# Kernel tuning notes

Measured on AMD Instinct MI355X. Metric: run time of the kernel, lower is better.

## Reference

```python
import jax, jax.numpy as jnp
import numpy as np

B, T, N, DIN = 16, 40, 64, 64
H = 256          # n_hid == msg_out == gru_hid (required by the module's own shape constraints)
MSG_HID = 256
DOUT = 64
E = N * (N - 1)  # fully-connected directed graph, no self loops


def _linear_params(key, fin, fout):
    kw, kb = jax.random.split(key)
    s = 1.0 / np.sqrt(fin)
    w = jax.random.uniform(kw, (fout, fin), minval=-s, maxval=s, dtype=jnp.float32)
    b = jax.random.uniform(kb, (fout,), minval=-s, maxval=s, dtype=jnp.float32)
    return w, b


def setup_inputs() -> dict:
    key = jax.random.key(0)
    ks = jax.random.split(key, 16)
    # one-hot incidence matrices for all ordered node pairs (i != j)
    pairs = np.array([(i, j) for i in range(N) for j in range(N) if i != j])
    eye = np.eye(N, dtype=np.float32)
    rel_send = jnp.asarray(eye[pairs[:, 0]])  # [E, N]
    rel_rec = jnp.asarray(eye[pairs[:, 1]])   # [E, N]

    inputs = jax.random.normal(ks[0], (B, T, N, DIN), dtype=jnp.float32)
    rel_types = jax.random.uniform(ks[1], (B, E, 2), dtype=jnp.float32)

    d = {"inputs": inputs, "rel_rec": rel_rec, "rel_send": rel_send, "rel_types": rel_types}
    names_dims = [
        ("msg_fc1", 2 * H, MSG_HID), ("msg_fc2", MSG_HID, H),
        ("gru_ir", DIN, H), ("gru_hr", H, H),
        ("gru_ii", DIN, H), ("gru_hi", H, H),
        ("gru_in", DIN, H), ("gru_hn", H, H),
        ("out_fc1", H, H), ("out_fc2", H, H), ("out_fc3", H, DOUT),
    ]
    for k, (name, fin, fout) in zip(ks[2:13], names_dims):
        w, b = _linear_params(k, fin, fout)
        d[name + "_w"] = w
        d[name + "_b"] = b
    return d


def _lin(x, w, b):
    return x @ w.T + b


def reference(inputs, rel_rec, rel_send, rel_types,
              msg_fc1_w, msg_fc1_b, msg_fc2_w, msg_fc2_b,
              gru_ir_w, gru_ir_b, gru_hr_w, gru_hr_b,
              gru_ii_w, gru_ii_b, gru_hi_w, gru_hi_b,
              gru_in_w, gru_in_b, gru_hn_w, gru_hn_b,
              out_fc1_w, out_fc1_b, out_fc2_w, out_fc2_b, out_fc3_w, out_fc3_b):
    b, t, n, _ = inputs.shape
    # both edge-type branches share the same message MLP, so the summed
    # message equals msg * (rel_types[...,0] + rel_types[...,1])
    type_sum = rel_types[:, :, 0:1] + rel_types[:, :, 1:2]  # [B, E, 1]

    def step(hidden, xt):
        # node2edge on hidden: [B, E, 2H]
        senders = jnp.einsum('en,bnh->beh', rel_send, hidden)
        receivers = jnp.einsum('en,bnh->beh', rel_rec, hidden)
        pre_msg = jnp.concatenate([senders, receivers], axis=-1)
        msg = jax.nn.relu(_lin(pre_msg, msg_fc1_w, msg_fc1_b))
        msg = jax.nn.relu(_lin(msg, msg_fc2_w, msg_fc2_b))
        all_msgs = msg * type_sum                                   # [B, E, H]
        agg_msgs = jnp.einsum('beh,en->bnh', all_msgs, rel_rec)     # edge2node
        r = jax.nn.sigmoid(_lin(xt, gru_ir_w, gru_ir_b) + _lin(agg_msgs, gru_hr_w, gru_hr_b))
        i = jax.nn.sigmoid(_lin(xt, gru_ii_w, gru_ii_b) + _lin(agg_msgs, gru_hi_w, gru_hi_b))
        nn_ = jnp.tanh(_lin(xt, gru_in_w, gru_in_b) + r * _lin(agg_msgs, gru_hn_w, gru_hn_b))
        hidden = (1.0 - i) * nn_ + i * hidden
        pred = jax.nn.relu(_lin(hidden, out_fc1_w, out_fc1_b))
        pred = jax.nn.relu(_lin(pred, out_fc2_w, out_fc2_b))
        pred = _lin(pred, out_fc3_w, out_fc3_b)
        return hidden, pred

    xs = jnp.transpose(inputs[:, :-1], (1, 0, 2, 3))  # time-major [T-1, B, N, DIN]
    h0 = jnp.zeros((b, n, H), dtype=inputs.dtype)
    _, preds = jax.lax.scan(step, h0, xs)
    return jnp.transpose(preds, (1, 0, 2, 3))          # [B, T-1, N, n_out]
```

## Files before the change

### kernel.cpp

```cpp
#include <hip/hip_runtime.h>
#include <math.h>


namespace {
constexpr int kB = 16, kT = 40, kTS = 39, kN = 64, kDin = 64, kH = 256;
constexpr int kE = kN * (kN - 1);
constexpr int kBN = kB * kN;
constexpr int kDout = 64;
}

typedef _Float16 half8 __attribute__((ext_vector_type(8)));
typedef short short8 __attribute__((ext_vector_type(8)));
typedef float f32x4 __attribute__((ext_vector_type(4)));

__device__ __forceinline__ float sigm(float x) { return 1.f / (1.f + expf(-x)); }

__device__ __forceinline__ unsigned short f2h(float x) {
    _Float16 h = (_Float16)x;
    return __builtin_bit_cast(unsigned short, h);
}

__device__ __forceinline__ uint4 pack8h(const float* x) {
    unsigned us[8];
    #pragma unroll
    for (int q = 0; q < 8; ++q) us[q] = f2h(x[q]);
    uint4 p;
    p.x = us[0] | (us[1] << 16); p.y = us[2] | (us[3] << 16);
    p.z = us[4] | (us[5] << 16); p.w = us[6] | (us[7] << 16);
    return p;
}

__global__ void setup_kernel(
    const float* __restrict__ rel_rec, const float* __restrict__ rel_send,
    const float* __restrict__ rel_types, const float* __restrict__ W2,
    const float* __restrict__ Whr, const float* __restrict__ Whi,
    const float* __restrict__ Whn, const float* __restrict__ Wir,
    const float* __restrict__ Wii, const float* __restrict__ Win,
    const float* __restrict__ W1,
    const float* __restrict__ bir, const float* __restrict__ bhr,
    const float* __restrict__ bii, const float* __restrict__ bhi,
    const float* __restrict__ fc1w, const float* __restrict__ fc2w,
    const float* __restrict__ fc3w,
    int* __restrict__ edge_at, float* __restrict__ ts,
    unsigned short* __restrict__ W2f,
    unsigned short* __restrict__ Wri,
    unsigned short* __restrict__ Wnh,
    unsigned short* __restrict__ Wnx,
    unsigned short* __restrict__ Wuv,
    unsigned short* __restrict__ F1, unsigned short* __restrict__ F2,
    unsigned short* __restrict__ F3,
    float* __restrict__ bri) {
    int idx = blockIdx.x * 256 + threadIdx.x;
    if (idx < kE) {
        int si = 0, ri = 0;
        for (int n = 0; n < kN; ++n) {
            if (rel_send[idx * kN + n] > 0.5f) si = n;
            if (rel_rec[idx * kN + n] > 0.5f) ri = n;
        }
        edge_at[ri * kN + si] = idx;
    }
    if (idx < kB * kE) ts[idx] = rel_types[2 * idx] + rel_types[2 * idx + 1];
    if (idx < kH * kH) {
        W2f[idx] = f2h(W2[idx]);
        Wnh[idx] = f2h(Whn[idx]);
        F1[idx] = f2h(fc1w[idx]);
        F2[idx] = f2h(fc2w[idx]);
    }
    if (idx < 512 * 320) {
        int row = idx / 320, k = idx - row * 320;
        float v;
        if (row < 256) v = (k < kH) ? Whr[row * kH + k] : Wir[row * kDin + k - kH];
        else { int o = row - 256; v = (k < kH) ? Whi[o * kH + k] : Wii[o * kDin + k - kH]; }
        Wri[idx] = f2h(v);
    }
    if (idx < kH * kDin) Wnx[idx] = f2h(Win[idx]);
    if (idx < 512 * 256) {
        int row = idx >> 8, k = idx & 255;
        float v = (row < 256) ? W1[row * 512 + k] : W1[(row - 256) * 512 + 256 + k];
        Wuv[idx] = f2h(v);
    }
    if (idx < kDout * kH) F3[idx] = f2h(fc3w[idx]);
    if (idx < 256) bri[idx] = bir[idx] + bhr[idx];
    else if (idx < 512) bri[idx] = bii[idx - 256] + bhi[idx - 256];
}

__global__ __launch_bounds__(512, 1)
void step_kernel(const float* __restrict__ hprev,
                 const float* __restrict__ inputs, int t,
                 const float* __restrict__ Uin, const float* __restrict__ Vin,
                 const unsigned short* __restrict__ W2f,
                 const float* __restrict__ b1, const float* __restrict__ b2,
                 const float* __restrict__ ts, const int* __restrict__ edge_at,
                 const unsigned short* __restrict__ Wri,
                 const unsigned short* __restrict__ Wnh,
                 const unsigned short* __restrict__ Wnx,
                 const unsigned short* __restrict__ Wuv,
                 const float* __restrict__ bri, const float* __restrict__ bhn,
                 const float* __restrict__ bin_,
                 float* __restrict__ hnew,
                 float* __restrict__ Uo, float* __restrict__ Vo,
                 unsigned short* __restrict__ hist16) {
    __shared__ __align__(16) unsigned short h1[kN * kH];
    __shared__ float vjb4[4][kH];
    __shared__ float tss4[4][kN];
    __shared__ float aggL[4][kH];
    __shared__ __align__(16) unsigned short Zf[16 * 320];
    __shared__ __align__(16) unsigned short Hf[16 * 256];

    const int tid = threadIdx.x;
    const int lane = tid & 63, w = tid >> 6;
    const int mrow = lane & 15, mq = lane >> 4;
    const int cb = ((blockIdx.x & 7) << 5) | (blockIdx.x >> 3);
    const int m0 = cb * 4;
    const int b = cb >> 4, j0 = (cb & 15) * 4;

    {
        const int jj = tid >> 7, o = tid & 127;
        const int j = j0 + jj;
        vjb4[jj][o] = Vin[(size_t)(b * kN + j) * kH + o] + b1[o];
        vjb4[jj][o + 128] = Vin[(size_t)(b * kN + j) * kH + o + 128] + b1[o + 128];
        if (o < kN) {
            int e = edge_at[j * kN + o];
            tss4[jj][o] = (e < 0) ? 0.f : ts[b * kE + e];
        }
    }

    const int uo = tid & 31, ui0 = tid >> 5;
    float ur[4][8];
    #pragma unroll
    for (int p = 0; p < 4; ++p) {
        const float4* up = (const float4*)(Uin + (size_t)(b * kN + ui0 + 16 * p) * kH + uo * 8);
        *(float4*)&ur[p][0] = up[0];
        *(float4*)&ur[p][4] = up[1];
    }

    const unsigned short* Wp = W2f + (size_t)(w * 32 + mrow) * kH + mq * 8;
    half8 bb[8][2];
    #pragma unroll
    for (int kt = 0; kt < 8; ++kt)
        #pragma unroll
        for (int nf = 0; nf < 2; ++nf)
            bb[kt][nf] = *(const half8*)(Wp + nf * 16 * kH + kt * 32);
    __builtin_amdgcn_sched_barrier(0);
    __syncthreads();

    #pragma unroll 1
    for (int jj = 0; jj < 4; ++jj) {
        const int j = j0 + jj;
        {
            const int k0 = uo * 8;
            float vj[8];
            *(float4*)&vj[0] = *(const float4*)&vjb4[jj][k0];
            *(float4*)&vj[4] = *(const float4*)&vjb4[jj][k0 + 4];
            #pragma unroll
            for (int p = 0; p < 4; ++p) {
                const int i = ui0 + 16 * p;
                float x[8];
                #pragma unroll
                for (int q = 0; q < 8; ++q)
                    x[q] = (i == j) ? 0.f : fmaxf(ur[p][q] + vj[q], 0.f);
                const int byte = i * 512 + ((k0 * 2) ^ ((i & 7) << 4));
                *(uint4*)((char*)h1 + byte) = pack8h(x);
            }
        }
        __syncthreads();

        f32x4 acc[4][2];
        #pragma unroll
        for (int mf = 0; mf < 4; ++mf)
            #pragma unroll
            for (int nf = 0; nf < 2; ++nf) acc[mf][nf] = (f32x4){0.f, 0.f, 0.f, 0.f};
        #pragma unroll
        for (int kt = 0; kt < 8; ++kt) {
            const int k0 = kt * 32;
            half8 a[4];
            #pragma unroll
            for (int mf = 0; mf < 4; ++mf) {
                const int r = mf * 16 + mrow;
                const int byte = r * 512 + (((k0 + mq * 8) * 2) ^ ((r & 7) << 4));
                a[mf] = *(const half8*)((const char*)h1 + byte);
            }
            #pragma unroll
            for (int mf = 0; mf < 4; ++mf)
                #pragma unroll
                for (int nf = 0; nf < 2; ++nf)
                    acc[mf][nf] = __builtin_amdgcn_mfma_f32_16x16x32_f16(
                        a[mf], bb[kt][nf], acc[mf][nf], 0, 0, 0);
        }

        float tsr[16];
        #pragma unroll
        for (int mf = 0; mf < 4; ++mf)
            #pragma unroll
            for (int r = 0; r < 4; ++r)
                tsr[mf * 4 + r] = tss4[jj][mf * 16 + mq * 4 + r];
        #pragma unroll
        for (int nf = 0; nf < 2; ++nf) {
            const int col = w * 32 + nf * 16 + mrow;
            const float bv = b2[col];
            float s = 0.f;
            #pragma unroll
            for (int mf = 0; mf < 4; ++mf)
                #pragma unroll
                for (int r = 0; r < 4; ++r)
                    s += tsr[mf * 4 + r] * fmaxf(acc[mf][nf][r] + bv, 0.f);
            s += __shfl_xor(s, 16);
            s += __shfl_xor(s, 32);
            if (lane < 16) aggL[jj][col] = s;
        }
        __syncthreads();
    }

    {
        const uint4 z4 = {0u, 0u, 0u, 0u};
        for (int c = tid; c < 4 * 40; c += 512) {
            const int r = c / 40, g = c - r * 40;
            float x[8];
            if (g < 32) {
                #pragma unroll
                for (int q = 0; q < 8; ++q) x[q] = aggL[r][g * 8 + q];
            } else {
                const int grow = m0 + r, bb_ = grow >> 6, n = grow & 63;
                const float* xp = inputs + ((size_t)(bb_ * kT + t) * kN + n) * kDin + (g - 32) * 8;
                *(float4*)&x[0] = ((const float4*)xp)[0];
                *(float4*)&x[4] = ((const float4*)xp)[1];
            }
            const int byte = r * 640 + ((g ^ (r & 7)) << 4);
            *(uint4*)((char*)Zf + byte) = pack8h(x);
        }
        for (int c = tid; c < 12 * 40; c += 512) {
            const int r = 4 + c / 40, g = c - (c / 40) * 40;
            const int byte = r * 640 + ((g ^ (r & 7)) << 4);
            *(uint4*)((char*)Zf + byte) = z4;
        }
        for (int c = tid; c < 12 * 32; c += 512) {
            const int r = 4 + c / 32, g = c & 31;
            const int byte = r * 512 + ((g ^ (r & 7)) << 4);
            *(uint4*)((char*)Hf + byte) = z4;
        }
    }
    __syncthreads();

    #pragma unroll
    for (int nf = 0; nf < 2; ++nf) {
        const int col = w * 32 + nf * 16 + mrow;
        const unsigned short* WR = Wri + (size_t)col * 320 + mq * 8;
        const unsigned short* WI = Wri + (size_t)(256 + col) * 320 + mq * 8;
        const unsigned short* WNh = Wnh + (size_t)col * kH + mq * 8;
        const unsigned short* WNx = Wnx + (size_t)col * kDin + mq * 8;

        half8 rwa[10][3];
        #pragma unroll
        for (int kt = 0; kt < 10; ++kt) {
            rwa[kt][0] = *(const half8*)(WR + kt * 32);
            rwa[kt][1] = *(const half8*)(WI + kt * 32);
            if (kt < 8) rwa[kt][2] = *(const half8*)(WNh + kt * 32);
            else        rwa[kt][2] = *(const half8*)(WNx + (kt * 32 - 256));
        }
        __builtin_amdgcn_sched_barrier(0);

        f32x4 aR = {0.f,0.f,0.f,0.f}, aI = {0.f,0.f,0.f,0.f};
        f32x4 aNH = {0.f,0.f,0.f,0.f}, aNX = {0.f,0.f,0.f,0.f};
        #pragma unroll
        for (int kt = 0; kt < 10; ++kt) {
            const int g = kt * 4 + mq;
            const int byte = mrow * 640 + ((g ^ (mrow & 7)) << 4);
            half8 zf = *(const half8*)((const char*)Zf + byte);
            aR = __builtin_amdgcn_mfma_f32_16x16x32_f16(zf, rwa[kt][0], aR, 0, 0, 0);
            aI = __builtin_amdgcn_mfma_f32_16x16x32_f16(zf, rwa[kt][1], aI, 0, 0, 0);
            if (kt < 8) aNH = __builtin_amdgcn_mfma_f32_16x16x32_f16(zf, rwa[kt][2], aNH, 0, 0, 0);
            else        aNX = __builtin_amdgcn_mfma_f32_16x16x32_f16(zf, rwa[kt][2], aNX, 0, 0, 0);
        }

        if (mq == 0) {
            const float brv = bri[col], biv = bri[256 + col];
            const float bhnv = bhn[col], binv = bin_[col];
            #pragma unroll
            for (int reg = 0; reg < 4; ++reg) {
                const int lr = reg;
                const int grow = m0 + lr;
                float rg = sigm(aR[reg] + brv);
                float ig = sigm(aI[reg] + biv);
                float ng = tanhf(aNX[reg] + binv + rg * (aNH[reg] + bhnv));
                float h2 = (1.f - ig) * ng + ig * hprev[(size_t)grow * kH + col];
                hnew[(size_t)grow * kH + col] = h2;
                const unsigned short hv = f2h(h2);
                __builtin_nontemporal_store(
                    hv, &hist16[((size_t)t * kBN + grow) * kH + col]);
                const int byte = lr * 512 + (((col >> 3) ^ (lr & 7)) << 4) + (col & 7) * 2;
                *(unsigned short*)((char*)Hf + byte) = hv;
            }
        }
    }
    __syncthreads();

    #pragma unroll
    for (int nf = 0; nf < 4; ++nf) {
        const int col = w * 64 + nf * 16 + mrow;
        const unsigned short* Wp2 = Wuv + (size_t)col * kH + mq * 8;
        half8 rwa[8];
        #pragma unroll
        for (int kt = 0; kt < 8; ++kt) rwa[kt] = *(const half8*)(Wp2 + kt * 32);
        __builtin_amdgcn_sched_barrier(0);
        f32x4 aUV = {0.f, 0.f, 0.f, 0.f};
        #pragma unroll
        for (int kt = 0; kt < 8; ++kt) {
            const int g = kt * 4 + mq;
            const int byte = mrow * 512 + ((g ^ (mrow & 7)) << 4);
            half8 zf = *(const half8*)((const char*)Hf + byte);
            aUV = __builtin_amdgcn_mfma_f32_16x16x32_f16(zf, rwa[kt], aUV, 0, 0, 0);
        }
        if (mq == 0) {
            #pragma unroll
            for (int reg = 0; reg < 4; ++reg) {
                const int grow = m0 + reg;
                const float v = aUV[reg];
                if (col < 256) Uo[(size_t)grow * kH + col] = v;
                else Vo[(size_t)grow * kH + col - 256] = v;
            }
        }
    }
}

__global__ __launch_bounds__(256, 2)
void out_kernel(const unsigned short* __restrict__ hist16,
                const unsigned short* __restrict__ F1,
                const unsigned short* __restrict__ F2,
                const unsigned short* __restrict__ F3,
                const float* __restrict__ fc1b, const float* __restrict__ fc2b,
                const float* __restrict__ fc3b, float* __restrict__ out) {
    __shared__ __align__(16) unsigned short Af[64 * 256];
    __shared__ __align__(16) unsigned short Bf[64 * 256];
    const int m0 = blockIdx.x * 64;
    const int tid = threadIdx.x;
    const int lane = tid & 63, w = tid >> 6;
    const int mrow = lane & 15, mq = lane >> 4;

    #pragma unroll
    for (int it = 0; it < 8; ++it) {
        const int c = tid + it * 256;
        const int r = c >> 5, o = c & 31;
        short8 v = *(const short8*)(hist16 + (size_t)(m0 + r) * kH + o * 8);
        const int byte = r * 512 + ((o << 4) ^ ((r & 7) << 4));
        *(short8*)((char*)Af + byte) = v;
    }
    __syncthreads();

    #define LAYER(SRC, WW, BIAS, DST)                                           \
    {                                                                           \
        const unsigned short* wb = WW + (size_t)(w * 64 + mrow) * kH + mq * 8;  \
        half8 wall[8][4];                                                       \
        _Pragma("unroll")                                                       \
        for (int kt = 0; kt < 8; ++kt)                                          \
            _Pragma("unroll")                                                   \
            for (int nf = 0; nf < 4; ++nf)                                      \
                wall[kt][nf] = *(const half8*)(wb + nf * 16 * kH + kt * 32);    \
        __builtin_amdgcn_sched_barrier(0);                                      \
        f32x4 acc[4][4];                                                        \
        _Pragma("unroll")                                                       \
        for (int m = 0; m < 4; ++m)                                             \
            _Pragma("unroll")                                                   \
            for (int nf = 0; nf < 4; ++nf) acc[m][nf] = (f32x4){0.f,0.f,0.f,0.f};\
        _Pragma("unroll")                                                       \
        for (int kt = 0; kt < 8; ++kt) {                                        \
            const int k0 = kt * 32;                                             \
            half8 zf[4];                                                        \
            _Pragma("unroll")                                                   \
            for (int m = 0; m < 4; ++m) {                                       \
                const int r = m * 16 + mrow;                                    \
                const int byte = r * 512 + (((k0 + mq * 8) * 2) ^ ((r & 7) << 4)); \
                zf[m] = *(const half8*)((const char*)SRC + byte);               \
            }                                                                   \
            _Pragma("unroll")                                                   \
            for (int m = 0; m < 4; ++m)                                         \
                _Pragma("unroll")                                               \
                for (int nf = 0; nf < 4; ++nf)                                  \
                    acc[m][nf] = __builtin_amdgcn_mfma_f32_16x16x32_f16(        \
                        zf[m], wall[kt][nf], acc[m][nf], 0, 0, 0);              \
        }                                                                       \
        _Pragma("unroll")                                                       \
        for (int m = 0; m < 4; ++m)                                             \
            _Pragma("unroll")                                                   \
            for (int nf = 0; nf < 4; ++nf) {                                    \
                const int col = w * 64 + nf * 16 + mrow;                        \
                const float bv = BIAS[col];                                     \
                _Pragma("unroll")                                               \
                for (int reg = 0; reg < 4; ++reg) {                             \
                    const int lr = m * 16 + mq * 4 + reg;                       \
                    float v = fmaxf(acc[m][nf][reg] + bv, 0.f);                 \
                    const int byte = lr * 512 + (((col >> 3) ^ (lr & 7)) << 4) + (col & 7) * 2; \
                    *(unsigned short*)((char*)DST + byte) = f2h(v);             \
                }                                                               \
            }                                                                   \
        __syncthreads();                                                        \
    }

    LAYER(Af, F1, fc1b, Bf)
    LAYER(Bf, F2, fc2b, Af)

    {
        const int row = w * 16 + mrow;
        const unsigned short* wb = F3 + (size_t)row * kH + mq * 8;
        half8 wall[8];
        #pragma unroll
        for (int kt = 0; kt < 8; ++kt) wall[kt] = *(const half8*)(wb + kt * 32);
        __builtin_amdgcn_sched_barrier(0);
        f32x4 acc[4];
        #pragma unroll
        for (int m = 0; m < 4; ++m) acc[m] = (f32x4){0.f, 0.f, 0.f, 0.f};
        #pragma unroll
        for (int kt = 0; kt < 8; ++kt) {
            const int k0 = kt * 32;
            half8 zf[4];
            #pragma unroll
            for (int m = 0; m < 4; ++m) {
                const int r = m * 16 + mrow;
                const int byte = r * 512 + (((k0 + mq * 8) * 2) ^ ((r & 7) << 4));
                zf[m] = *(const half8*)((const char*)Af + byte);
            }
            #pragma unroll
            for (int m = 0; m < 4; ++m)
                acc[m] = __builtin_amdgcn_mfma_f32_16x16x32_f16(zf[m], wall[kt], acc[m], 0, 0, 0);
        }
        const int col = w * 16 + mrow;
        const float bv = fc3b[col];
        #pragma unroll
        for (int m = 0; m < 4; ++m)
            #pragma unroll
            for (int reg = 0; reg < 4; ++reg) {
                const int grow = m0 + m * 16 + mq * 4 + reg;
                const int t = grow >> 10, bn = grow & 1023, b = bn >> 6, n = bn & 63;
                out[(((size_t)b * kTS + t) * kN + n) * kDout + col] = acc[m][reg] + bv;
            }
    }
    #undef LAYER
}

extern "C" void kernel_launch(void* const* d_in, const int* in_sizes, int n_in,
                              void* d_out, int out_size, void* d_ws, size_t ws_size,
                              hipStream_t stream) {
    const float* inputs    = (const float*)d_in[0];
    const float* rel_rec   = (const float*)d_in[1];
    const float* rel_send  = (const float*)d_in[2];
    const float* rel_types = (const float*)d_in[3];
    const float* W1  = (const float*)d_in[4];  const float* b1  = (const float*)d_in[5];
    const float* W2  = (const float*)d_in[6];  const float* b2  = (const float*)d_in[7];
    const float* Wir = (const float*)d_in[8];  const float* bir = (const float*)d_in[9];
    const float* Whr = (const float*)d_in[10]; const float* bhr = (const float*)d_in[11];
    const float* Wii = (const float*)d_in[12]; const float* bii = (const float*)d_in[13];
    const float* Whi = (const float*)d_in[14]; const float* bhi = (const float*)d_in[15];
    const float* Win = (const float*)d_in[16]; const float* bin_ = (const float*)d_in[17];
    const float* Whn = (const float*)d_in[18]; const float* bhn = (const float*)d_in[19];
    const float* fc1w = (const float*)d_in[20]; const float* fc1b = (const float*)d_in[21];
    const float* fc2w = (const float*)d_in[22]; const float* fc2b = (const float*)d_in[23];
    const float* fc3w = (const float*)d_in[24]; const float* fc3b = (const float*)d_in[25];
    float* out = (float*)d_out;

    char* w = (char*)d_ws;
    auto take = [&](size_t bytes) { char* p = w; w += (bytes + 255) & ~(size_t)255; return p; };
    int* edge_at = (int*)take(kN * kN * 4);
    float* ts = (float*)take(kB * kE * 4);
    unsigned short* W2f = (unsigned short*)take(kH * kH * 2);
    unsigned short* Wri = (unsigned short*)take(512 * 320 * 2);
    unsigned short* Wnh = (unsigned short*)take(kH * kH * 2);
    unsigned short* Wnx = (unsigned short*)take(kH * kDin * 2);
    unsigned short* Wuv = (unsigned short*)take(512 * 256 * 2);
    unsigned short* F1 = (unsigned short*)take(kH * kH * 2);
    unsigned short* F2 = (unsigned short*)take(kH * kH * 2);
    unsigned short* F3 = (unsigned short*)take(kDout * kH * 2);
    float* bri = (float*)take(512 * 4);
    float* Ua = (float*)take((size_t)kBN * kH * 4);
    float* Va = (float*)take((size_t)kBN * kH * 4);
    float* Ub = (float*)take((size_t)kBN * kH * 4);
    float* Vb = (float*)take((size_t)kBN * kH * 4);
    float* ha = (float*)take((size_t)kBN * kH * 4);
    float* hb_ = (float*)take((size_t)kBN * kH * 4);
    unsigned short* hist16 = (unsigned short*)take((size_t)kTS * kBN * kH * 2);

    hipMemsetAsync(edge_at, 0xFF, kN * kN * 4, stream);
    setup_kernel<<<640, 256, 0, stream>>>(
        rel_rec, rel_send, rel_types, W2, Whr, Whi, Whn, Wir, Wii, Win, W1,
        bir, bhr, bii, bhi, fc1w, fc2w, fc3w,
        edge_at, ts, W2f, Wri, Wnh, Wnx, Wuv, F1, F2, F3, bri);
    hipMemsetAsync(Ua, 0, (size_t)kBN * kH * 4, stream);
    hipMemsetAsync(Va, 0, (size_t)kBN * kH * 4, stream);
    hipMemsetAsync(ha, 0, (size_t)kBN * kH * 4, stream);

    float* Uc = Ua; float* Vc = Va; float* Un = Ub; float* Vn = Vb;
    float* hc = ha; float* hn = hb_;
    for (int t = 0; t < kTS; ++t) {
        step_kernel<<<kBN / 4, 512, 0, stream>>>(
            hc, inputs, t, Uc, Vc,
            W2f, b1, b2, ts, edge_at, Wri, Wnh, Wnx, Wuv, bri, bhn, bin_,
            hn, Un, Vn, hist16);
        float* tmp;
        tmp = Uc; Uc = Un; Un = tmp;
        tmp = Vc; Vc = Vn; Vn = tmp;
        tmp = hc; hc = hn; hn = tmp;
    }
    out_kernel<<<kTS * kBN / 64, 256, 0, stream>>>(
        hist16, F1, F2, F3, fc1b, fc2b, fc3b, out);
}
```

Measured before the change: 1.555 ms.

## Double step kernel block to 1024 threads, processing two receiver nodes per round

```diff
diff --git a/kernel.cpp b/kernel.cpp
--- a/kernel.cpp
+++ b/kernel.cpp
@@ -84,7 +84,7 @@
     else if (idx < 512) bri[idx] = bii[idx - 256] + bhi[idx - 256];
 }
 
-__global__ __launch_bounds__(512, 1)
+__global__ __launch_bounds__(1024, 1)
 void step_kernel(const float* __restrict__ hprev,
                  const float* __restrict__ inputs, int t,
                  const float* __restrict__ Uin, const float* __restrict__ Vin,
@@ -100,7 +100,7 @@
                  float* __restrict__ hnew,
                  float* __restrict__ Uo, float* __restrict__ Vo,
                  unsigned short* __restrict__ hist16) {
-    __shared__ __align__(16) unsigned short h1[kN * kH];
+    __shared__ __align__(16) unsigned short h1[2][kN * kH];
     __shared__ float vjb4[4][kH];
     __shared__ float tss4[4][kN];
     __shared__ float aggL[4][kH];
@@ -115,17 +115,18 @@
     const int b = cb >> 4, j0 = (cb & 15) * 4;
 
     {
-        const int jj = tid >> 7, o = tid & 127;
+        const int jj = tid >> 8, o = tid & 255;
         const int j = j0 + jj;
         vjb4[jj][o] = Vin[(size_t)(b * kN + j) * kH + o] + b1[o];
-        vjb4[jj][o + 128] = Vin[(size_t)(b * kN + j) * kH + o + 128] + b1[o + 128];
         if (o < kN) {
             int e = edge_at[j * kN + o];
             tss4[jj][o] = (e < 0) ? 0.f : ts[b * kE + e];
         }
     }
 
-    const int uo = tid & 31, ui0 = tid >> 5;
+    const int pb = tid >> 9;
+    const int tl = tid & 511;
+    const int uo = tl & 31, ui0 = tl >> 5;
     float ur[4][8];
     #pragma unroll
     for (int p = 0; p < 4; ++p) {
@@ -134,7 +135,8 @@
         *(float4*)&ur[p][4] = up[1];
     }
 
-    const unsigned short* Wp = W2f + (size_t)(w * 32 + mrow) * kH + mq * 8;
+    const int wcol = w & 7, wpb = w >> 3;
+    const unsigned short* Wp = W2f + (size_t)(wcol * 32 + mrow) * kH + mq * 8;
     half8 bb[8][2];
     #pragma unroll
     for (int kt = 0; kt < 8; ++kt)
@@ -142,16 +144,28 @@
         for (int nf = 0; nf < 2; ++nf)
             bb[kt][nf] = *(const half8*)(Wp + nf * 16 * kH + kt * 32);
     __builtin_amdgcn_sched_barrier(0);
+
+    {
+        const uint4 z4 = {0u, 0u, 0u, 0u};
+        for (int c = tid; c < 12 * 40; c += 1024) {
+            const int r = 4 + c / 40, g = c - (c / 40) * 40;
+            *(uint4*)((char*)Zf + r * 640 + ((g ^ (r & 7)) << 4)) = z4;
+        }
+        for (int c = tid; c < 12 * 32; c += 1024) {
+            const int r = 4 + c / 32, g = c & 31;
+            *(uint4*)((char*)Hf + r * 512 + ((g ^ (r & 7)) << 4)) = z4;
+        }
+    }
     __syncthreads();
 
     #pragma unroll 1
-    for (int jj = 0; jj < 4; ++jj) {
-        const int j = j0 + jj;
+    for (int round = 0; round < 2; ++round) {
         {
+            const int j = j0 + 2 * round + pb;
             const int k0 = uo * 8;
             float vj[8];
-            *(float4*)&vj[0] = *(const float4*)&vjb4[jj][k0];
-            *(float4*)&vj[4] = *(const float4*)&vjb4[jj][k0 + 4];
+            *(float4*)&vj[0] = *(const float4*)&vjb4[2 * round + pb][k0];
+            *(float4*)&vj[4] = *(const float4*)&vjb4[2 * round + pb][k0 + 4];
             #pragma unroll
             for (int p = 0; p < 4; ++p) {
                 const int i = ui0 + 16 * p;
@@ -159,12 +173,12 @@
                 #pragma unroll
                 for (int q = 0; q < 8; ++q)
                     x[q] = (i == j) ? 0.f : fmaxf(ur[p][q] + vj[q], 0.f);
-                const int byte = i * 512 + ((k0 * 2) ^ ((i & 7) << 4));
-                *(uint4*)((char*)h1 + byte) = pack8h(x);
+                *(uint4*)((char*)h1[pb] + i * 512 + ((k0 * 2) ^ ((i & 7) << 4))) = pack8h(x);
             }
         }
         __syncthreads();
 
+        const int jj = 2 * round + wpb;
         f32x4 acc[4][2];
         #pragma unroll
         for (int mf = 0; mf < 4; ++mf)
@@ -177,8 +191,8 @@
             #pragma unroll
             for (int mf = 0; mf < 4; ++mf) {
                 const int r = mf * 16 + mrow;
-                const int byte = r * 512 + (((k0 + mq * 8) * 2) ^ ((r & 7) << 4));
-                a[mf] = *(const half8*)((const char*)h1 + byte);
+                a[mf] = *(const half8*)((const char*)h1[wpb] + r * 512 +
+                                        (((k0 + mq * 8) * 2) ^ ((r & 7) << 4)));
             }
             #pragma unroll
             for (int mf = 0; mf < 4; ++mf)
@@ -196,7 +210,7 @@
                 tsr[mf * 4 + r] = tss4[jj][mf * 16 + mq * 4 + r];
         #pragma unroll
         for (int nf = 0; nf < 2; ++nf) {
-            const int col = w * 32 + nf * 16 + mrow;
+            const int col = wcol * 32 + nf * 16 + mrow;
             const float bv = b2[col];
             float s = 0.f;
             #pragma unroll
@@ -211,39 +225,24 @@
         __syncthreads();
     }
 
+    for (int c = tid; c < 4 * 40; c += 1024) {
+        const int r = c / 40, g = c - r * 40;
+        float x[8];
+        if (g < 32) {
+            #pragma unroll
+            for (int q = 0; q < 8; ++q) x[q] = aggL[r][g * 8 + q];
+        } else {
+            const int grow = m0 + r, bb_ = grow >> 6, n = grow & 63;
+            const float* xp = inputs + ((size_t)(bb_ * kT + t) * kN + n) * kDin + (g - 32) * 8;
+            *(float4*)&x[0] = ((const float4*)xp)[0];
+            *(float4*)&x[4] = ((const float4*)xp)[1];
+        }
+        *(uint4*)((char*)Zf + r * 640 + ((g ^ (r & 7)) << 4)) = pack8h(x);
+    }
+    __syncthreads();
+
     {
-        const uint4 z4 = {0u, 0u, 0u, 0u};
-        for (int c = tid; c < 4 * 40; c += 512) {
-            const int r = c / 40, g = c - r * 40;
-            float x[8];
-            if (g < 32) {
-                #pragma unroll
-                for (int q = 0; q < 8; ++q) x[q] = aggL[r][g * 8 + q];
-            } else {
-                const int grow = m0 + r, bb_ = grow >> 6, n = grow & 63;
-                const float* xp = inputs + ((size_t)(bb_ * kT + t) * kN + n) * kDin + (g - 32) * 8;
-                *(float4*)&x[0] = ((const float4*)xp)[0];
-                *(float4*)&x[4] = ((const float4*)xp)[1];
-            }
-            const int byte = r * 640 + ((g ^ (r & 7)) << 4);
-            *(uint4*)((char*)Zf + byte) = pack8h(x);
-        }
-        for (int c = tid; c < 12 * 40; c += 512) {
-            const int r = 4 + c / 40, g = c - (c / 40) * 40;
-            const int byte = r * 640 + ((g ^ (r & 7)) << 4);
-            *(uint4*)((char*)Zf + byte) = z4;
-        }
-        for (int c = tid; c < 12 * 32; c += 512) {
-            const int r = 4 + c / 32, g = c & 31;
-            const int byte = r * 512 + ((g ^ (r & 7)) << 4);
-            *(uint4*)((char*)Hf + byte) = z4;
-        }
-    }
-    __syncthreads();
-
-    #pragma unroll
-    for (int nf = 0; nf < 2; ++nf) {
-        const int col = w * 32 + nf * 16 + mrow;
+        const int col = w * 16 + mrow;
         const unsigned short* WR = Wri + (size_t)col * 320 + mq * 8;
         const unsigned short* WI = Wri + (size_t)(256 + col) * 320 + mq * 8;
         const unsigned short* WNh = Wnh + (size_t)col * kH + mq * 8;
@@ -264,8 +263,7 @@
         #pragma unroll
         for (int kt = 0; kt < 10; ++kt) {
             const int g = kt * 4 + mq;
-            const int byte = mrow * 640 + ((g ^ (mrow & 7)) << 4);
-            half8 zf = *(const half8*)((const char*)Zf + byte);
+            half8 zf = *(const half8*)((const char*)Zf + mrow * 640 + ((g ^ (mrow & 7)) << 4));
             aR = __builtin_amdgcn_mfma_f32_16x16x32_f16(zf, rwa[kt][0], aR, 0, 0, 0);
             aI = __builtin_amdgcn_mfma_f32_16x16x32_f16(zf, rwa[kt][1], aI, 0, 0, 0);
             if (kt < 8) aNH = __builtin_amdgcn_mfma_f32_16x16x32_f16(zf, rwa[kt][2], aNH, 0, 0, 0);
@@ -277,8 +275,7 @@
             const float bhnv = bhn[col], binv = bin_[col];
             #pragma unroll
             for (int reg = 0; reg < 4; ++reg) {
-                const int lr = reg;
-                const int grow = m0 + lr;
+                const int grow = m0 + reg;
                 float rg = sigm(aR[reg] + brv);
                 float ig = sigm(aI[reg] + biv);
                 float ng = tanhf(aNX[reg] + binv + rg * (aNH[reg] + bhnv));
@@ -287,16 +284,16 @@
                 const unsigned short hv = f2h(h2);
                 __builtin_nontemporal_store(
                     hv, &hist16[((size_t)t * kBN + grow) * kH + col]);
-                const int byte = lr * 512 + (((col >> 3) ^ (lr & 7)) << 4) + (col & 7) * 2;
-                *(unsigned short*)((char*)Hf + byte) = hv;
+                *(unsigned short*)((char*)Hf + reg * 512 +
+                    (((col >> 3) ^ (reg & 7)) << 4) + (col & 7) * 2) = hv;
             }
         }
     }
     __syncthreads();
 
     #pragma unroll
-    for (int nf = 0; nf < 4; ++nf) {
-        const int col = w * 64 + nf * 16 + mrow;
+    for (int nf = 0; nf < 2; ++nf) {
+        const int col = w * 32 + nf * 16 + mrow;
         const unsigned short* Wp2 = Wuv + (size_t)col * kH + mq * 8;
         half8 rwa[8];
         #pragma unroll
@@ -306,8 +303,7 @@
         #pragma unroll
         for (int kt = 0; kt < 8; ++kt) {
             const int g = kt * 4 + mq;
-            const int byte = mrow * 512 + ((g ^ (mrow & 7)) << 4);
-            half8 zf = *(const half8*)((const char*)Hf + byte);
+            half8 zf = *(const half8*)((const char*)Hf + mrow * 512 + ((g ^ (mrow & 7)) << 4));
             aUV = __builtin_amdgcn_mfma_f32_16x16x32_f16(zf, rwa[kt], aUV, 0, 0, 0);
         }
         if (mq == 0) {
@@ -489,7 +485,7 @@
     float* Uc = Ua; float* Vc = Va; float* Un = Ub; float* Vn = Vb;
     float* hc = ha; float* hn = hb_;
     for (int t = 0; t < kTS; ++t) {
-        step_kernel<<<kBN / 4, 512, 0, stream>>>(
+        step_kernel<<<kBN / 4, 1024, 0, stream>>>(
             hc, inputs, t, Uc, Vc,
             W2f, b1, b2, ts, edge_at, Wri, Wnh, Wnx, Wuv, bri, bhn, bin_,
             hn, Un, Vn, hist16);
```

After: 3.125 ms. 2.01x slower.
